# Kernel tuning notes

Measured on AMD Instinct MI355X. Metric: run time of the kernel, lower is better.

The kernel has to match this reference:

```python
import jax, jax.numpy as jnp
import numpy as np
from jax import lax

N = 63        # fixed by ConvTranspose chain: 3->5->9->17->33->63
ML = 3        # smoother mid channels
KS = 7        # smoother kernel size
MID = 32      # hypernet mid channels
K_ITERS = 5   # outer solver iterations
B = 256


def _conv2d(x, w, pad):
    return lax.conv_general_dilated(x, w, (1, 1), [(pad, pad), (pad, pad)],
                                    dimension_numbers=('NCHW', 'OIHW', 'NCHW'))


def _batch_conv2d(x, kernels):
    # per-sample 3x3 stencil conv via grouped conv: x [B,1,m,m], kernels [B,1,3,3]
    b, _, m1, m2 = x.shape
    out = lax.conv_general_dilated(x.reshape(1, b, m1, m2), kernels, (1, 1),
                                   [(0, 0), (0, 0)],
                                   dimension_numbers=('NCHW', 'OIHW', 'NCHW'),
                                   feature_group_count=b)
    return out.reshape(b, 1, m1 - 2, m2 - 2)


def _conv_transpose2d(x, w, b, stride, padding):
    # torch ConvTranspose2d: w layout [in, out, k, k]
    k = w.shape[-1]
    w2 = jnp.flip(w, (-2, -1)).transpose(1, 0, 2, 3)  # [out, in, k, k]
    p = k - 1 - padding
    y = lax.conv_general_dilated(x, w2, (1, 1), [(p, p), (p, p)],
                                 lhs_dilation=(stride, stride),
                                 dimension_numbers=('NCHW', 'OIHW', 'NCHW'))
    return y + b[None, :, None, None]


def _pad_bc(x):
    # F.pad (1,0,1,0) with 0 then (0,1,0,1) with 1
    x = jnp.pad(x, ((0, 0), (0, 0), (1, 0), (1, 0)))
    return jnp.pad(x, ((0, 0), (0, 0), (0, 1), (0, 1)), constant_values=1.0)


def _gelu(x):
    return jax.nn.gelu(x, approximate=False)  # torch nn.GELU default is exact


def setup_inputs() -> dict:
    key = jax.random.key(0)
    ks = jax.random.split(key, 24)
    s = 0.02
    d = {}
    d['x'] = jax.random.normal(ks[0], (B, 1, N, N), jnp.float32)
    d['f'] = jax.random.normal(ks[1], (B, 1, N, N), jnp.float32)
    d['kernelA'] = jax.random.normal(ks[2], (B, 1, 3, 3), jnp.float32)
    # smoother hypernetwork (two Linear(9->100->mL*ks*ks) stacks)
    d['fc1_w1'] = jax.random.normal(ks[3], (9, 100), jnp.float32) * s
    d['fc1_b1'] = jnp.zeros((100,), jnp.float32)
    d['fc1_w2'] = jax.random.normal(ks[4], (100, ML * KS * KS), jnp.float32) * s
    d['fc1_b2'] = jnp.zeros((ML * KS * KS,), jnp.float32)
    d['fc2_w1'] = jax.random.normal(ks[5], (9, 100), jnp.float32) * s
    d['fc2_b1'] = jnp.zeros((100,), jnp.float32)
    d['fc2_w2'] = jax.random.normal(ks[6], (100, ML * KS * KS), jnp.float32) * s
    d['fc2_b2'] = jnp.zeros((ML * KS * KS,), jnp.float32)
    # CNNFNS meta: 5 ConvTranspose2d layers (torch weight layout [in,out,k,k])
    d['ct1_w'] = jax.random.normal(ks[7], (1, MID, 3, 3), jnp.float32) * s
    d['ct1_b'] = jnp.zeros((MID,), jnp.float32)
    d['ct2_w'] = jax.random.normal(ks[8], (MID, MID, 3, 3), jnp.float32) * s
    d['ct2_b'] = jnp.zeros((MID,), jnp.float32)
    d['ct3_w'] = jax.random.normal(ks[9], (MID, MID, 3, 3), jnp.float32) * s
    d['ct3_b'] = jnp.zeros((MID,), jnp.float32)
    d['ct4_w'] = jax.random.normal(ks[10], (MID, MID, 3, 3), jnp.float32) * s
    d['ct4_b'] = jnp.zeros((MID,), jnp.float32)
    d['ct5_w'] = jax.random.normal(ks[11], (MID, 2, 3, 3), jnp.float32) * s
    d['ct5_b'] = jnp.zeros((2,), jnp.float32)
    return d


def reference(x, f, kernelA,
              fc1_w1, fc1_b1, fc1_w2, fc1_b2,
              fc2_w1, fc2_b1, fc2_w2, fc2_b2,
              ct1_w, ct1_b, ct2_w, ct2_b, ct3_w, ct3_b, ct4_w, ct4_b, ct5_w, ct5_b):
    bsz = x.shape[0]

    # --- hypernet weights depend only on kernelA: hoist out of the K loop ---
    flatA = kernelA.reshape(bsz, 9)
    w1 = (_gelu(flatA @ fc1_w1 + fc1_b1) @ fc1_w2 + fc1_b2).reshape(bsz, ML, 1, KS, KS)
    w2 = (_gelu(flatA @ fc2_w1 + fc2_b1) @ fc2_w2 + fc2_b2).reshape(bsz, 1, ML, KS, KS)

    h = _gelu(_conv_transpose2d(kernelA, ct1_w, ct1_b, 2, 1))
    h = _gelu(_conv_transpose2d(h, ct2_w, ct2_b, 2, 1))
    h = _gelu(_conv_transpose2d(h, ct3_w, ct3_b, 2, 1))
    h = _gelu(_conv_transpose2d(h, ct4_w, ct4_b, 2, 1))
    h = _conv_transpose2d(h, ct5_w, ct5_b, 2, 2)          # [B,2,N,N]
    hw = h.reshape(bsz, 1, N, N, 2)                        # memory-reinterp view as in torch
    wc = lax.complex(hw[..., 0], hw[..., 1])               # [B,1,N,N] complex

    def residual(xc):
        return f - _batch_conv2d(_pad_bc(xc), kernelA)

    def smoother(xc):
        r = residual(xc)
        def per(r_i, a_i, b_i):
            t = _conv2d(r_i[None], a_i, KS // 2)           # [1,ML,N,N]
            return _conv2d(t, b_i, KS // 2)[0]             # [1,N,N]
        g2 = jax.vmap(per)(r, w1, w2)
        return xc + g2

    def h_correct(r):
        r_hat = jnp.fft.fft2(r, norm='ortho')
        out_ft = r_hat * wc
        # torch irfft2(s=(N,N)) trims last dim to N//2+1
        return jnp.fft.irfft2(out_ft[..., : N // 2 + 1], s=(N, N), norm='ortho')

    for _ in range(K_ITERS):
        x = smoother(x)
        x = x + h_correct(residual(x))
    r = residual(x)
    return jnp.linalg.norm(r) / bsz
```

## Files before the change

### kernel.cpp

```cpp
#include <hip/hip_runtime.h>
#include <math.h>

#define NB   256
#define ND   63
#define NN   3969

__device__ __forceinline__ float gelu_f(float v){
    return 0.5f * v * (1.0f + erff(v * 0.70710678118654752440f));
}

#define FMA4(A, W, S) { (A).x=fmaf((W).x,(S),(A).x); (A).y=fmaf((W).y,(S),(A).y); \
                        (A).z=fmaf((W).z,(S),(A).z); (A).w=fmaf((W).w,(S),(A).w); }

union F4  { float4 v;    float a[4];  };
union W16 { float4 v[4]; float a[16]; };

__device__ __forceinline__ float4 gelu4(const F4& x){
    float4 r;
    r.x = gelu_f(x.a[0]); r.y = gelu_f(x.a[1]);
    r.z = gelu_f(x.a[2]); r.w = gelu_f(x.a[3]);
    return r;
}

__device__ __forceinline__ int dec_base(int uc, int H){
    int h2 = H >> 1;
    return (uc < h2) ? 4*uc : (uc < H) ? 4*(uc - h2) + 1 : 2*H;
}

template<int SIN, int SOUT, int OST>
__device__ __forceinline__ void ct_quad_stage(const float* __restrict__ cin,
                                              float* __restrict__ cout,
                                              const float* __restrict__ wb,
                                              const float* __restrict__ bsv,
                                              int tid){
    const int H  = (SOUT - 1) >> 1;
    const int UX = H + 1;
    const int NU = UX * UX * 8;
    for (int u = tid; u < NU; u += 512){
        const int cell = u >> 3, q = u & 7;
        const int ucy = cell / UX, ucx = cell - ucy*UX;
        const int oy = dec_base(ucy, H), ox = dec_base(ucx, H);
        const bool vx = (ox + 2 <= 2*H), vy = (oy + 2 <= 2*H);
        int nky, kyA[2], iyA[2];
        if (oy & 1){ nky=2; kyA[0]=0; iyA[0]=(oy+1)>>1; kyA[1]=2; iyA[1]=(oy-1)>>1; }
        else       { nky=1; kyA[0]=1; iyA[0]=oy>>1; kyA[1]=1; iyA[1]=0; }
        int nkx, kxA[2], ixA[2];
        if (ox & 1){ nkx=2; kxA[0]=0; ixA[0]=(ox+1)>>1; kxA[1]=2; ixA[1]=(ox-1)>>1; }
        else       { nkx=1; kxA[0]=1; ixA[0]=ox>>1; kxA[1]=1; ixA[1]=0; }
        F4 a00, a01, a10, a11;
        a00.v = ((const float4*)bsv)[q]; a01.v = a00.v; a10.v = a00.v; a11.v = a00.v;
        for (int yi = 0; yi < nky; yi++)
        for (int xi = 0; xi < nkx; xi++){
            const float* wp  = wb + (kyA[yi]*3 + kxA[xi])*1024 + 4*q;
            const float* p00 = cin + (iyA[yi]*SIN + ixA[xi])*36;
            const float* p01 = p00 + 36;
            const float* p10 = p00 + SIN*36;
            const float* p11 = p10 + 36;
            #pragma unroll
            for (int g = 0; g < 8; g++){
                F4 i00, i01, i10, i11;
                i00.v = *(const float4*)(p00 + 4*g);
                i01.v = *(const float4*)(p01 + 4*g);
                i10.v = *(const float4*)(p10 + 4*g);
                i11.v = *(const float4*)(p11 + 4*g);
                #pragma unroll
                for (int cc = 0; cc < 4; cc++){
                    float4 w = *(const float4*)(wp + (4*g + cc)*32);
                    FMA4(a00.v, w, i00.a[cc]);
                    FMA4(a01.v, w, i01.a[cc]);
                    FMA4(a10.v, w, i10.a[cc]);
                    FMA4(a11.v, w, i11.a[cc]);
                }
            }
        }
        float4 g00 = gelu4(a00), g01 = gelu4(a01), g10 = gelu4(a10), g11 = gelu4(a11);
        size_t base = (size_t)(oy*SOUT + ox)*OST + 4*q;
        *(float4*)(cout + base) = g00;
        if (vx)        *(float4*)(cout + base + 2*(size_t)OST) = g01;
        if (vy)        *(float4*)(cout + base + 2*(size_t)SOUT*OST) = g10;
        if (vx && vy)  *(float4*)(cout + base + 2*(size_t)(SOUT+1)*OST) = g11;
    }
}

__global__ __launch_bounds__(512) void k_ct1234(const float* __restrict__ kA,
                                                const float* __restrict__ cw1,
                                                const float* __restrict__ cw2,
                                                const float* __restrict__ cw3,
                                                const float* __restrict__ cw4,
                                                const float* __restrict__ b1,
                                                const float* __restrict__ b2,
                                                const float* __restrict__ b3,
                                                const float* __restrict__ b4,
                                                float* __restrict__ c4out,
                                                float* __restrict__ acc){
    __shared__ __align__(16) float wbuf[9216];
    __shared__ __align__(16) float w1s[288];
    __shared__ __align__(16) float c1s[31*36];
    __shared__ __align__(16) float c2s[91*36];
    __shared__ __align__(16) float c3s[307*36];
    __shared__ float b1s[32], b2s[32], b3s[32], b4s[32];
    const int b = blockIdx.x, tid = threadIdx.x;
    if (b == 0 && tid == 0) acc[0] = 0.f;
    for (int i = tid; i < 9216; i += 512){
        int ci = i / 288, co = (i / 9) & 31, tap = i % 9;
        wbuf[tap*1024 + ci*32 + co] = cw2[i];
    }
    if (tid < 288) w1s[(tid % 9)*32 + tid/9] = cw1[tid];
    if (tid < 32){ b1s[tid]=b1[tid]; b2s[tid]=b2[tid]; b3s[tid]=b3[tid]; b4s[tid]=b4[tid]; }
    __syncthreads();
    if (tid < 200){
        int px = tid >> 3, q = tid & 7;
        int oy = px / 5, ox = px % 5;
        F4 a4; a4.v = ((const float4*)b1s)[q];
        int nky, kyA[2], iyA[2];
        if (oy & 1){ nky=2; kyA[0]=0; iyA[0]=(oy+1)/2; kyA[1]=2; iyA[1]=(oy-1)/2; }
        else       { nky=1; kyA[0]=1; iyA[0]=oy/2; kyA[1]=1; iyA[1]=0; }
        int nkx, kxA[2], ixA[2];
        if (ox & 1){ nkx=2; kxA[0]=0; ixA[0]=(ox+1)/2; kxA[1]=2; ixA[1]=(ox-1)/2; }
        else       { nkx=1; kxA[0]=1; ixA[0]=ox/2; kxA[1]=1; ixA[1]=0; }
        const float* ab = kA + b*9;
        for (int yi = 0; yi < nky; yi++)
        for (int xi = 0; xi < nkx; xi++){
            float v = ab[iyA[yi]*3 + ixA[xi]];
            float4 w = *(const float4*)(w1s + (kyA[yi]*3 + kxA[xi])*32 + 4*q);
            FMA4(a4.v, w, v);
        }
        *(float4*)(c1s + px*36 + 4*q) = gelu4(a4);
    }
    __syncthreads();
    ct_quad_stage<5, 9, 36>(c1s, c2s, wbuf, b2s, tid);
    __syncthreads();
    for (int i = tid; i < 9216; i += 512){
        int ci = i / 288, co = (i / 9) & 31, tap = i % 9;
        wbuf[tap*1024 + ci*32 + co] = cw3[i];
    }
    __syncthreads();
    ct_quad_stage<9, 17, 36>(c2s, c3s, wbuf, b3s, tid);
    __syncthreads();
    for (int i = tid; i < 9216; i += 512){
        int ci = i / 288, co = (i / 9) & 31, tap = i % 9;
        wbuf[tap*1024 + ci*32 + co] = cw4[i];
    }
    __syncthreads();
    ct_quad_stage<17, 33, 32>(c3s, c4out + (size_t)b*(1089*32), wbuf, b4s, tid);
}

__global__ __launch_bounds__(512) void k_solve(const float* __restrict__ x0g,
                                               const float* __restrict__ f,
                                               const float* __restrict__ kAg,
                                               const float* __restrict__ w1a, const float* __restrict__ b1a,
                                               const float* __restrict__ w2a, const float* __restrict__ b2a,
                                               const float* __restrict__ w1b, const float* __restrict__ b1b,
                                               const float* __restrict__ w2b, const float* __restrict__ b2b,
                                               const float* __restrict__ cw5,
                                               const float* __restrict__ b5,
                                               const float* __restrict__ c4g,
                                               float* __restrict__ accg){
    __shared__ __align__(16) float xs[63*68 + 8];
    __shared__ __align__(16) float U[17152 + 8];
    __shared__ __align__(16) float Fs_r[4288];
    __shared__ __align__(16) float Fs_i[4288];
    __shared__ __align__(16) float vcs[4096];
    __shared__ float ws5b[576];
    __shared__ float w1s[148], w2s[148], dvs[64], ds_r[32], ds_i[32], red[8], hs[100];
    const int b = blockIdx.x, tid = threadIdx.x;
    float* rs  = U;
    float* tc0 = U + 4288;
    float* tc1 = U + 8576;
    float* tc2 = U + 12864;
    float*  rP  = U;
    const float4* rP4 = (const float4*)U;
    float2* TtC = (float2*)(U + 4096);
    float2* MC2 = (float2*)U;
    float4* CC4 = (float4*)(U + 4096);
    float* c5s = U;
    const float4* F4r = (const float4*)Fs_r;
    const float4* F4i = (const float4*)Fs_i;
    const float4* vc4s = (const float4*)vcs;
    const float* fg = f + (size_t)b*NN;
    float ka[9];
    #pragma unroll
    for (int i = 0; i < 9; i++) ka[i] = kAg[b*9 + i];

    for (int i = tid; i < 4288; i += 512){
        int r = i / 68, c = i % 68;
        float vr = 0.f, vi = 0.f;
        if (r < 63 && c < 63){
            int m = (r * c) % 63;
            float ang = 6.283185307179586f * (float)m / 63.0f;
            vr = cosf(ang); vi = -sinf(ang);
        }
        Fs_r[i] = vr; Fs_i[i] = vi;
    }
    for (int i = tid; i < 576; i += 512){
        int ci = i / 18, co = (i / 9) & 1, tap = i % 9;
        ws5b[tap*64 + ci*2 + co] = cw5[i];
    }
    for (int i = tid; i < NN; i += 512) xs[(i/ND)*68 + (i%ND)] = x0g[(size_t)b*NN + i];
    if (tid < 100){
        float s = b1a[tid];
        #pragma unroll
        for (int i = 0; i < 9; i++) s = fmaf(ka[i], w1a[i*100 + tid], s);
        hs[tid] = gelu_f(s);
    }
    __syncthreads();
    if (tid < 147){
        float s = b2a[tid];
        for (int k = 0; k < 100; k++) s = fmaf(hs[k], w2a[k*147 + tid], s);
        w1s[tid] = s;
    }
    __syncthreads();
    if (tid < 100){
        float s = b1b[tid];
        #pragma unroll
        for (int i = 0; i < 9; i++) s = fmaf(ka[i], w1b[i*100 + tid], s);
        hs[tid] = gelu_f(s);
    }
    __syncthreads();
    if (tid < 147){
        float s = b2b[tid];
        for (int k = 0; k < 100; k++) s = fmaf(hs[k], w2b[k*147 + tid], s);
        w2s[tid] = s;
    }
    {
        const float* ib = c4g + (size_t)b * (1089*32);
        float bb0 = b5[0], bb1 = b5[1];
        for (int p = tid; p < NN; p += 512){
            int oy = p / ND, ox = p % ND;
            float a0 = bb0, a1 = bb1;
            int nky, kyA[2], iyA[2];
            if ((oy & 1) == 0){ nky=2; kyA[0]=0; iyA[0]=oy/2+1; kyA[1]=2; iyA[1]=oy/2; }
            else              { nky=1; kyA[0]=1; iyA[0]=(oy+1)/2; kyA[1]=1; iyA[1]=0; }
            int nkx, kxA[2], ixA[2];
            if ((ox & 1) == 0){ nkx=2; kxA[0]=0; ixA[0]=ox/2+1; kxA[1]=2; ixA[1]=ox/2; }
            else              { nkx=1; kxA[0]=1; ixA[0]=(ox+1)/2; kxA[1]=1; ixA[1]=0; }
            for (int yi = 0; yi < nky; yi++)
            for (int xi = 0; xi < nkx; xi++){
                const float* ip = ib + ((size_t)iyA[yi]*33 + ixA[xi])*32;
                const float* wp = ws5b + (kyA[yi]*3 + kxA[xi])*64;
                #pragma unroll
                for (int g = 0; g < 8; g++){
                    F4 iv; iv.v = *(const float4*)(ip + 4*g);
                    #pragma unroll
                    for (int q = 0; q < 4; q++){
                        int ci = 4*g + q;
                        a0 = fmaf(iv.a[q], wp[ci*2],   a0);
                        a1 = fmaf(iv.a[q], wp[ci*2+1], a1);
                    }
                }
            }
            c5s[p]      = a0;
            c5s[NN + p] = a1;
        }
    }
    __syncthreads();
    {
        const float sc = 1.0f / 3969.0f;
        float4* vout = (float4*)vcs;
        for (int i = tid; i < 1024; i += 512){
            int ky = i >> 5, ct2 = i & 31;
            float4 o;
            #pragma unroll
            for (int j = 0; j < 2; j++){
                int kx = 2*ct2 + j;
                float re = 0.f, im = 0.f;
                if (kx <= 31){ int o2 = 2*(ky*ND + kx); re = c5s[o2]*sc; im = c5s[o2+1]*sc; }
                else if (kx <= 62){
                    int sy = (ND - ky) % ND, sx = ND - kx;
                    int o2 = 2*(sy*ND + sx); re = c5s[o2]*sc; im = -c5s[o2+1]*sc;
                }
                if (j == 0){ o.x = re; o.y = im; } else { o.z = re; o.w = im; }
            }
            vout[i] = o;
        }
        if (tid < 32){
            float2 d = {0.f, 0.f};
            if (tid >= 1){
                int iA = (ND - tid) * ND, iB = tid * ND;
                d.x = (c5s[2*iA]     - c5s[2*iB])     * sc;
                d.y = (c5s[2*iA + 1] + c5s[2*iB + 1]) * sc;
            }
            ((float2*)dvs)[tid] = d;
        }
    }
    __syncthreads();

    const int kt = tid >> 4, cg = tid & 15;

    for (int it = 0; it < 5; it++){
        for (int i = tid; i < NN; i += 512){
            int y = i / ND, xx = i % ND;
            float s = 0.f;
            #pragma unroll
            for (int dy = 0; dy < 3; dy++){
                int u = y + dy;
                #pragma unroll
                for (int dx = 0; dx < 3; dx++){
                    int v = xx + dx;
                    float p;
                    if (u == 64 || v == 64)    p = 1.0f;
                    else if (u == 0 || v == 0) p = 0.0f;
                    else                       p = xs[(u-1)*68 + (v-1)];
                    s = fmaf(p, ka[dy*3 + dx], s);
                }
            }
            rs[y*68 + 3 + xx] = fg[i] - s;
        }
        for (int i = tid; i < 1276; i += 512){
            int buf = i / 319, j = i - buf*319;
            float* base = U + buf*4288;
            int idx;
            if (j < 315){ int rr = j/5, cc = j - rr*5; idx = rr*68 + ((cc < 3) ? cc : 63 + cc); }
            else idx = 4284 + (j - 315);
            base[idx] = 0.f;
        }
        __syncthreads();
        const bool act = tid < 504;
        const int y0 = tid >> 3, x0c = 8*(tid & 7);
        if (act){
            float A0[8] = {}, A1[8] = {}, A2[8] = {};
            for (int dy = 0; dy < 7; dy++){
                int ry = y0 + dy - 3;
                if (ry < 0 || ry >= 63) continue;
                W16 w16;
                const float4* rp = (const float4*)(rs + ry*68 + x0c);
                w16.v[0]=rp[0]; w16.v[1]=rp[1]; w16.v[2]=rp[2]; w16.v[3]=rp[3];
                #pragma unroll
                for (int dx = 0; dx < 7; dx++){
                    float w0 = w1s[dy*7 + dx];
                    float w1 = w1s[49 + dy*7 + dx];
                    float w2 = w1s[98 + dy*7 + dx];
                    #pragma unroll
                    for (int t = 0; t < 8; t++){
                        float v = w16.a[t+dx];
                        A0[t] = fmaf(w0, v, A0[t]);
                        A1[t] = fmaf(w1, v, A1[t]);
                        A2[t] = fmaf(w2, v, A2[t]);
                    }
                }
            }
            int nw = 63 - x0c; if (nw > 8) nw = 8;
            for (int t = 0; t < nw; t++){
                int o = y0*68 + 3 + x0c + t;
                tc0[o] = A0[t]; tc1[o] = A1[t]; tc2[o] = A2[t];
            }
        }
        __syncthreads();
        if (act){
            float acc2[8] = {};
            #pragma unroll
            for (int c = 0; c < 3; c++){
                const float* tcc = (c == 0) ? tc0 : (c == 1) ? tc1 : tc2;
                for (int dy = 0; dy < 7; dy++){
                    int ry = y0 + dy - 3;
                    if (ry < 0 || ry >= 63) continue;
                    W16 w16;
                    const float4* tp = (const float4*)(tcc + ry*68 + x0c);
                    w16.v[0]=tp[0]; w16.v[1]=tp[1]; w16.v[2]=tp[2]; w16.v[3]=tp[3];
                    #pragma unroll
                    for (int dx = 0; dx < 7; dx++){
                        float wv = w2s[c*49 + dy*7 + dx];
                        #pragma unroll
                        for (int t = 0; t < 8; t++) acc2[t] = fmaf(wv, w16.a[t+dx], acc2[t]);
                    }
                }
            }
            int nw = 63 - x0c; if (nw > 8) nw = 8;
            for (int t = 0; t < nw; t++) xs[y0*68 + x0c + t] += acc2[t];
        }
        __syncthreads();
        for (int i = tid; i < 4096; i += 512){
            int y = i >> 6, xx = i & 63;
            float val = 0.f;
            if (y < 63 && xx < 63){
                float s = 0.f;
                #pragma unroll
                for (int dy = 0; dy < 3; dy++){
                    int u = y + dy;
                    #pragma unroll
                    for (int dx = 0; dx < 3; dx++){
                        int v = xx + dx;
                        float p;
                        if (u == 64 || v == 64)    p = 1.0f;
                        else if (u == 0 || v == 0) p = 0.0f;
                        else                       p = xs[(u-1)*68 + (v-1)];
                        s = fmaf(p, ka[dy*3 + dx], s);
                    }
                }
                val = fg[y*ND + xx] - s;
            }
            rP[i] = val;
        }
        __syncthreads();
        {
            float tr0=0.f,ti0=0.f,tr1=0.f,ti1=0.f,tr2=0.f,ti2=0.f,tr3=0.f,ti3=0.f;
            for (int mq = 0; mq < 16; mq++){
                F4 f4r, f4i;
                f4r.v = F4r[kt*17 + mq];
                f4i.v = F4i[kt*17 + mq];
                #pragma unroll
                for (int j = 0; j < 4; j++){
                    F4 rv; rv.v = rP4[(4*mq + j)*16 + cg];
                    float fr = f4r.a[j], fi = f4i.a[j];
                    tr0 = fmaf(fr, rv.a[0], tr0); ti0 = fmaf(fi, rv.a[0], ti0);
                    tr1 = fmaf(fr, rv.a[1], tr1); ti1 = fmaf(fi, rv.a[1], ti1);
                    tr2 = fmaf(fr, rv.a[2], tr2); ti2 = fmaf(fi, rv.a[2], ti2);
                    tr3 = fmaf(fr, rv.a[3], tr3); ti3 = fmaf(fi, rv.a[3], ti3);
                }
            }
            const int c0 = 4*cg;
            TtC[(c0+0)*32 + ((kt + c0 + 0) & 31)] = make_float2(tr0, ti0);
            TtC[(c0+1)*32 + ((kt + c0 + 1) & 31)] = make_float2(tr1, ti1);
            TtC[(c0+2)*32 + ((kt + c0 + 2) & 31)] = make_float2(tr2, ti2);
            TtC[(c0+3)*32 + ((kt + c0 + 3) & 31)] = make_float2(tr3, ti3);
        }
        __syncthreads();
        {
            float R0r,R0i,R1r,R1i,R2r,R2i,R3r,R3i;
            {
                float2 T0 = TtC[kt & 31];
                R0r = T0.x; R0i = T0.y;
                R1r = T0.x; R1i = T0.y;
                R2r = T0.x; R2i = T0.y;
                R3r = T0.x; R3i = T0.y;
            }
            for (int np = 1; np <= 31; np++){
                int n2 = 63 - np;
                float2 T1 = TtC[np*32 + ((kt + np) & 31)];
                float2 T2 = TtC[n2*32 + ((kt + n2) & 31)];
                F4 fr, fi;
                fr.v = F4r[np*17 + cg];
                fi.v = F4i[np*17 + cg];
                float Sx = T1.x + T2.x, Dx = T1.x - T2.x;
                float Sy = T1.y + T2.y, Dy = T2.y - T1.y;
                R0r = fmaf(fr.a[0], Sx, R0r); R0r = fmaf(fi.a[0], Dy, R0r);
                R0i = fmaf(fi.a[0], Dx, R0i); R0i = fmaf(fr.a[0], Sy, R0i);
                R1r = fmaf(fr.a[1], Sx, R1r); R1r = fmaf(fi.a[1], Dy, R1r);
                R1i = fmaf(fi.a[1], Dx, R1i); R1i = fmaf(fr.a[1], Sy, R1i);
                R2r = fmaf(fr.a[2], Sx, R2r); R2r = fmaf(fi.a[2], Dy, R2r);
                R2i = fmaf(fi.a[2], Dx, R2i); R2i = fmaf(fr.a[2], Sy, R2i);
                R3r = fmaf(fr.a[3], Sx, R3r); R3r = fmaf(fi.a[3], Dy, R3r);
                R3i = fmaf(fi.a[3], Dx, R3i); R3i = fmaf(fr.a[3], Sy, R3i);
            }
            if (cg == 0){
                float2 dv = ((const float2*)dvs)[kt];
                ds_r[kt] = R0r*dv.x + R0i*dv.y;
                ds_i[kt] = R0r*dv.y - R0i*dv.x;
            }
            float4 vA = vc4s[kt*32 + 2*cg];
            float4 vB = vc4s[kt*32 + 2*cg + 1];
            const int c0 = 4*cg, rot = kt;
            MC2[kt*64 + ((c0+0 + rot) & 63)] = make_float2(R0r*vA.x - R0i*vA.y, R0r*vA.y + R0i*vA.x);
            MC2[kt*64 + ((c0+1 + rot) & 63)] = make_float2(R1r*vA.z - R1i*vA.w, R1r*vA.w + R1i*vA.z);
            MC2[kt*64 + ((c0+2 + rot) & 63)] = make_float2(R2r*vB.x - R2i*vB.y, R2r*vB.y + R2i*vB.x);
            MC2[kt*64 + ((c0+3 + rot) & 63)] = make_float2(R3r*vB.z - R3i*vB.w, R3r*vB.w + R3i*vB.z);
        }
        __syncthreads();
        {
            const int rot = kt;
            float C0r,C0i,C1r,C1i,C2r,C2i,C3r,C3i;
            {
                float2 M0 = MC2[kt*64 + (rot & 63)];
                C0r = M0.x; C0i = M0.y;
                C1r = M0.x; C1i = M0.y;
                C2r = M0.x; C2i = M0.y;
                C3r = M0.x; C3i = M0.y;
            }
            for (int lp = 1; lp <= 31; lp++){
                int l2 = 63 - lp;
                float2 M1 = MC2[kt*64 + ((lp + rot) & 63)];
                float2 M2 = MC2[kt*64 + ((l2 + rot) & 63)];
                F4 fr, fi;
                fr.v = F4r[lp*17 + cg];
                fi.v = F4i[lp*17 + cg];
                float SMx = M1.x + M2.x, DMx = M2.x - M1.x;
                float SMy = M1.y + M2.y, DMy = M1.y - M2.y;
                C0r = fmaf(fr.a[0], SMx, C0r); C0r = fmaf(fi.a[0], DMy, C0r);
                C0i = fmaf(fr.a[0], SMy, C0i); C0i = fmaf(fi.a[0], DMx, C0i);
                C1r = fmaf(fr.a[1], SMx, C1r); C1r = fmaf(fi.a[1], DMy, C1r);
                C1i = fmaf(fr.a[1], SMy, C1i); C1i = fmaf(fi.a[1], DMx, C1i);
                C2r = fmaf(fr.a[2], SMx, C2r); C2r = fmaf(fi.a[2], DMy, C2r);
                C2i = fmaf(fr.a[2], SMy, C2i); C2i = fmaf(fi.a[2], DMx, C2i);
                C3r = fmaf(fr.a[3], SMx, C3r); C3r = fmaf(fi.a[3], DMy, C3r);
                C3i = fmaf(fr.a[3], SMy, C3i); C3i = fmaf(fi.a[3], DMx, C3i);
            }
            float sc2 = (kt == 0) ? 0.5f : 1.0f;
            CC4[kt*33 + 2*cg]     = make_float4(C0r*sc2, C0i*sc2, C1r*sc2, C1i*sc2);
            CC4[kt*33 + 2*cg + 1] = make_float4(C2r*sc2, C2i*sc2, C3r*sc2, C3i*sc2);
        }
        __syncthreads();
        if (tid < 256){
            const int pr = tid >> 3, qb = tid & 7;
            float sr[8] = {}, si[8] = {};
            float er = 0.f, ei = 0.f;
            for (int nq = 0; nq < 8; nq++){
                F4 f4r, f4i;
                f4r.v = F4r[pr*17 + nq];
                f4i.v = F4i[pr*17 + nq];
                #pragma unroll
                for (int j = 0; j < 4; j++){
                    int n = 4*nq + j;
                    float fr = f4r.a[j], fi = f4i.a[j];
                    float4 cA = CC4[n*33 + qb];
                    float4 cB = CC4[n*33 + qb + 8];
                    float4 cC = CC4[n*33 + qb + 16];
                    float4 cD = CC4[n*33 + qb + 24];
                    sr[0]=fmaf(fr,cA.x,sr[0]); si[0]=fmaf(fi,cA.y,si[0]);
                    sr[1]=fmaf(fr,cA.z,sr[1]); si[1]=fmaf(fi,cA.w,si[1]);
                    sr[2]=fmaf(fr,cB.x,sr[2]); si[2]=fmaf(fi,cB.y,si[2]);
                    sr[3]=fmaf(fr,cB.z,sr[3]); si[3]=fmaf(fi,cB.w,si[3]);
                    sr[4]=fmaf(fr,cC.x,sr[4]); si[4]=fmaf(fi,cC.y,si[4]);
                    sr[5]=fmaf(fr,cC.z,sr[5]); si[5]=fmaf(fi,cC.w,si[5]);
                    sr[6]=fmaf(fr,cD.x,sr[6]); si[6]=fmaf(fi,cD.y,si[6]);
                    sr[7]=fmaf(fr,cD.z,sr[7]); si[7]=fmaf(fi,cD.w,si[7]);
                    er = fmaf(fr, ds_r[n], er); ei = fmaf(fi, ds_i[n], ei);
                }
            }
            {
                float e0 = er - ei;
                float* xrow = xs + pr*68;
                float2* xp0 = (float2*)(xrow + 2*qb);
                float2* xp1 = (float2*)(xrow + 2*qb + 16);
                float2* xp2 = (float2*)(xrow + 2*qb + 32);
                float2* xp3 = (float2*)(xrow + 2*qb + 48);
                float2 v0=*xp0, v1=*xp1, v2=*xp2, v3=*xp3;
                v0.x += 2.f*(sr[0]+si[0]) + e0; v0.y += 2.f*(sr[1]+si[1]) + e0;
                v1.x += 2.f*(sr[2]+si[2]) + e0; v1.y += 2.f*(sr[3]+si[3]) + e0;
                v2.x += 2.f*(sr[4]+si[4]) + e0; v2.y += 2.f*(sr[5]+si[5]) + e0;
                v3.x += 2.f*(sr[6]+si[6]) + e0; v3.y += 2.f*(sr[7]+si[7]) + e0;
                *xp0=v0; *xp1=v1; *xp2=v2; *xp3=v3;
            }
            if (pr > 0){
                float e1 = er + ei;
                float* xrow = xs + (63-pr)*68;
                float2* xp0 = (float2*)(xrow + 2*qb);
                float2* xp1 = (float2*)(xrow + 2*qb + 16);
                float2* xp2 = (float2*)(xrow + 2*qb + 32);
                float2* xp3 = (float2*)(xrow + 2*qb + 48);
                float2 v0=*xp0, v1=*xp1, v2=*xp2, v3=*xp3;
                v0.x += 2.f*(sr[0]-si[0]) + e1; v0.y += 2.f*(sr[1]-si[1]) + e1;
                v1.x += 2.f*(sr[2]-si[2]) + e1; v1.y += 2.f*(sr[3]-si[3]) + e1;
                v2.x += 2.f*(sr[4]-si[4]) + e1; v2.y += 2.f*(sr[5]-si[5]) + e1;
                v3.x += 2.f*(sr[6]-si[6]) + e1; v3.y += 2.f*(sr[7]-si[7]) + e1;
                *xp0=v0; *xp1=v1; *xp2=v2; *xp3=v3;
            }
        }
        __syncthreads();
    }
    float s = 0.f;
    for (int i = tid; i < NN; i += 512){
        int y = i / ND, xx = i % ND;
        float cv = 0.f;
        #pragma unroll
        for (int dy = 0; dy < 3; dy++){
            int u = y + dy;
            #pragma unroll
            for (int dx = 0; dx < 3; dx++){
                int v = xx + dx;
                float p;
                if (u == 64 || v == 64)    p = 1.0f;
                else if (u == 0 || v == 0) p = 0.0f;
                else                       p = xs[(u-1)*68 + (v-1)];
                cv = fmaf(p, ka[dy*3 + dx], cv);
            }
        }
        float r = fg[i] - cv;
        s = fmaf(r, r, s);
    }
    #pragma unroll
    for (int off = 32; off > 0; off >>= 1) s += __shfl_down(s, off, 64);
    int lane = tid & 63, w = tid >> 6;
    if (lane == 0) red[w] = s;
    __syncthreads();
    if (tid == 0){
        float t = 0.f;
        #pragma unroll
        for (int i = 0; i < 8; i++) t += red[i];
        atomicAdd(accg, t);
    }
}

__global__ void k_final(const float* __restrict__ acc, float* __restrict__ out){
    if (threadIdx.x == 0 && blockIdx.x == 0) out[0] = sqrtf(acc[0]) * (1.0f/256.0f);
}

extern "C" void kernel_launch(void* const* d_in, const int* in_sizes, int n_in,
                              void* d_out, int out_size, void* d_ws, size_t ws_size,
                              hipStream_t stream){
    const float* x0     = (const float*)d_in[0];
    const float* f      = (const float*)d_in[1];
    const float* kA     = (const float*)d_in[2];
    const float* fc1_w1 = (const float*)d_in[3];
    const float* fc1_b1 = (const float*)d_in[4];
    const float* fc1_w2 = (const float*)d_in[5];
    const float* fc1_b2 = (const float*)d_in[6];
    const float* fc2_w1 = (const float*)d_in[7];
    const float* fc2_b1 = (const float*)d_in[8];
    const float* fc2_w2 = (const float*)d_in[9];
    const float* fc2_b2 = (const float*)d_in[10];
    const float* ct1_w  = (const float*)d_in[11];
    const float* ct1_b  = (const float*)d_in[12];
    const float* ct2_w  = (const float*)d_in[13];
    const float* ct2_b  = (const float*)d_in[14];
    const float* ct3_w  = (const float*)d_in[15];
    const float* ct3_b  = (const float*)d_in[16];
    const float* ct4_w  = (const float*)d_in[17];
    const float* ct4_b  = (const float*)d_in[18];
    const float* ct5_w  = (const float*)d_in[19];
    const float* ct5_b  = (const float*)d_in[20];
    float* out = (float*)d_out;

    float* ws = (float*)d_ws;
    size_t off = 0;
    auto take = [&](size_t n){ float* p = ws + off; off += (n + 63) & ~(size_t)63; return p; };
    float* acc = take(64);
    float* c4  = take((size_t)NB*32*1089);
    (void)ws_size; (void)in_sizes; (void)n_in; (void)out_size;

    k_ct1234<<<NB, 512, 0, stream>>>(kA, ct1_w, ct2_w, ct3_w, ct4_w,
                                     ct1_b, ct2_b, ct3_b, ct4_b, c4, acc);
    k_solve<<<NB, 512, 0, stream>>>(x0, f, kA,
                                    fc1_w1, fc1_b1, fc1_w2, fc1_b2,
                                    fc2_w1, fc2_b1, fc2_w2, fc2_b2,
                                    ct5_w, ct5_b, c4, acc);
    k_final<<<1, 64, 0, stream>>>(acc, out);
}
```

Baseline: 353.3 us.

## Pad solution tile with boundary halo and exploit row symmetry in DFT stage

Stores the solution in a shared buffer with a baked-in halo (zeros on top/left, ones on bottom/right), so the 3x3 residual stencils become branch-free, vectorized 8-wide register sweeps reusing float4 row loads. All residual computations, including the final norm, switch to this tiled form. The first DFT stage also pairs rows m and 63-m, using cos/sin symmetry to roughly halve its multiply-adds. The cost is a larger shared array and remapped indexing that must stay consistent with the halo layout.

```diff
diff --git a/kernel.cpp b/kernel.cpp
--- a/kernel.cpp
+++ b/kernel.cpp
@@ -156,7 +156,7 @@
                                                const float* __restrict__ b5,
                                                const float* __restrict__ c4g,
                                                float* __restrict__ accg){
-    __shared__ __align__(16) float xs[63*68 + 8];
+    __shared__ __align__(16) float xs[65*68 + 8];
     __shared__ __align__(16) float U[17152 + 8];
     __shared__ __align__(16) float Fs_r[4288];
     __shared__ __align__(16) float Fs_i[4288];
@@ -192,11 +192,16 @@
         }
         Fs_r[i] = vr; Fs_i[i] = vi;
     }
+    for (int i = tid; i < 4428; i += 512){
+        int r = i / 68, c = i - r*68;
+        bool interior = (r >= 1 && r <= 63 && c >= 4 && c <= 66);
+        if (!interior) xs[i] = (r == 64 || c == 67) ? 1.f : 0.f;
+    }
     for (int i = tid; i < 576; i += 512){
         int ci = i / 18, co = (i / 9) & 1, tap = i % 9;
         ws5b[tap*64 + ci*2 + co] = cw5[i];
     }
-    for (int i = tid; i < NN; i += 512) xs[(i/ND)*68 + (i%ND)] = x0g[(size_t)b*NN + i];
+    for (int i = tid; i < NN; i += 512) xs[(i/ND + 1)*68 + (i%ND) + 4] = x0g[(size_t)b*NN + i];
     if (tid < 100){
         float s = b1a[tid];
         #pragma unroll
@@ -286,25 +291,27 @@
     __syncthreads();
 
     const int kt = tid >> 4, cg = tid & 15;
+    const bool act = tid < 504;
+    const int y0 = tid >> 3, xc = 8*(tid & 7);
 
     for (int it = 0; it < 5; it++){
-        for (int i = tid; i < NN; i += 512){
-            int y = i / ND, xx = i % ND;
-            float s = 0.f;
+        if (act){
+            float racc[8] = {};
             #pragma unroll
             for (int dy = 0; dy < 3; dy++){
-                int u = y + dy;
+                W16 w;
+                const float4* rp = (const float4*)(xs + (y0 + dy)*68 + xc);
+                w.v[0]=rp[0]; w.v[1]=rp[1]; w.v[2]=rp[2]; w.v[3]=rp[3];
                 #pragma unroll
                 for (int dx = 0; dx < 3; dx++){
-                    int v = xx + dx;
-                    float p;
-                    if (u == 64 || v == 64)    p = 1.0f;
-                    else if (u == 0 || v == 0) p = 0.0f;
-                    else                       p = xs[(u-1)*68 + (v-1)];
-                    s = fmaf(p, ka[dy*3 + dx], s);
-                }
-            }
-            rs[y*68 + 3 + xx] = fg[i] - s;
+                    float kv = ka[dy*3 + dx];
+                    #pragma unroll
+                    for (int t = 0; t < 8; t++) racc[t] = fmaf(kv, w.a[3 + t + dx], racc[t]);
+                }
+            }
+            int nw = 63 - xc; if (nw > 8) nw = 8;
+            const float* fr_ = fg + y0*ND + xc;
+            for (int t = 0; t < nw; t++) rs[y0*68 + 3 + xc + t] = fr_[t] - racc[t];
         }
         for (int i = tid; i < 1276; i += 512){
             int buf = i / 319, j = i - buf*319;
@@ -315,15 +322,13 @@
             base[idx] = 0.f;
         }
         __syncthreads();
-        const bool act = tid < 504;
-        const int y0 = tid >> 3, x0c = 8*(tid & 7);
         if (act){
             float A0[8] = {}, A1[8] = {}, A2[8] = {};
             for (int dy = 0; dy < 7; dy++){
                 int ry = y0 + dy - 3;
                 if (ry < 0 || ry >= 63) continue;
                 W16 w16;
-                const float4* rp = (const float4*)(rs + ry*68 + x0c);
+                const float4* rp = (const float4*)(rs + ry*68 + xc);
                 w16.v[0]=rp[0]; w16.v[1]=rp[1]; w16.v[2]=rp[2]; w16.v[3]=rp[3];
                 #pragma unroll
                 for (int dx = 0; dx < 7; dx++){
@@ -339,9 +344,9 @@
                     }
                 }
             }
-            int nw = 63 - x0c; if (nw > 8) nw = 8;
+            int nw = 63 - xc; if (nw > 8) nw = 8;
             for (int t = 0; t < nw; t++){
-                int o = y0*68 + 3 + x0c + t;
+                int o = y0*68 + 3 + xc + t;
                 tc0[o] = A0[t]; tc1[o] = A1[t]; tc2[o] = A2[t];
             }
         }
@@ -355,7 +360,7 @@
                     int ry = y0 + dy - 3;
                     if (ry < 0 || ry >= 63) continue;
                     W16 w16;
-                    const float4* tp = (const float4*)(tcc + ry*68 + x0c);
+                    const float4* tp = (const float4*)(tcc + ry*68 + xc);
                     w16.v[0]=tp[0]; w16.v[1]=tp[1]; w16.v[2]=tp[2]; w16.v[3]=tp[3];
                     #pragma unroll
                     for (int dx = 0; dx < 7; dx++){
@@ -365,49 +370,63 @@
                     }
                 }
             }
-            int nw = 63 - x0c; if (nw > 8) nw = 8;
-            for (int t = 0; t < nw; t++) xs[y0*68 + x0c + t] += acc2[t];
-        }
-        __syncthreads();
-        for (int i = tid; i < 4096; i += 512){
-            int y = i >> 6, xx = i & 63;
-            float val = 0.f;
-            if (y < 63 && xx < 63){
-                float s = 0.f;
+            int nw = 63 - xc; if (nw > 8) nw = 8;
+            for (int t = 0; t < nw; t++) xs[(y0+1)*68 + 4 + xc + t] += acc2[t];
+        }
+        __syncthreads();
+        if (act){
+            float racc[8] = {};
+            #pragma unroll
+            for (int dy = 0; dy < 3; dy++){
+                W16 w;
+                const float4* rp = (const float4*)(xs + (y0 + dy)*68 + xc);
+                w.v[0]=rp[0]; w.v[1]=rp[1]; w.v[2]=rp[2]; w.v[3]=rp[3];
                 #pragma unroll
-                for (int dy = 0; dy < 3; dy++){
-                    int u = y + dy;
+                for (int dx = 0; dx < 3; dx++){
+                    float kv = ka[dy*3 + dx];
                     #pragma unroll
-                    for (int dx = 0; dx < 3; dx++){
-                        int v = xx + dx;
-                        float p;
-                        if (u == 64 || v == 64)    p = 1.0f;
-                        else if (u == 0 || v == 0) p = 0.0f;
-                        else                       p = xs[(u-1)*68 + (v-1)];
-                        s = fmaf(p, ka[dy*3 + dx], s);
-                    }
-                }
-                val = fg[y*ND + xx] - s;
-            }
-            rP[i] = val;
+                    for (int t = 0; t < 8; t++) racc[t] = fmaf(kv, w.a[3 + t + dx], racc[t]);
+                }
+            }
+            float out[8];
+            #pragma unroll
+            for (int t = 0; t < 8; t++){
+                int ci = xc + t; if (ci > 62) ci = 62;
+                float fv = fg[y0*ND + ci];
+                out[t] = (xc + t < 63) ? (fv - racc[t]) : 0.f;
+            }
+            *(float4*)(rP + y0*64 + xc)     = make_float4(out[0],out[1],out[2],out[3]);
+            *(float4*)(rP + y0*64 + xc + 4) = make_float4(out[4],out[5],out[6],out[7]);
         }
         __syncthreads();
         {
-            float tr0=0.f,ti0=0.f,tr1=0.f,ti1=0.f,tr2=0.f,ti2=0.f,tr3=0.f,ti3=0.f;
-            for (int mq = 0; mq < 16; mq++){
+            float tr0,ti0=0.f,tr1,ti1=0.f,tr2,ti2=0.f,tr3,ti3=0.f;
+            { F4 rv; rv.v = rP4[cg]; tr0=rv.a[0]; tr1=rv.a[1]; tr2=rv.a[2]; tr3=rv.a[3]; }
+            #define A_PAIR(MM, JJ) { \
+                F4 r1, r2; \
+                r1.v = rP4[(MM)*16 + cg]; \
+                r2.v = rP4[(63-(MM))*16 + cg]; \
+                float fr = f4r.a[JJ], fi = f4i.a[JJ]; \
+                float S0=r1.a[0]+r2.a[0], D0=r1.a[0]-r2.a[0]; \
+                float S1=r1.a[1]+r2.a[1], D1=r1.a[1]-r2.a[1]; \
+                float S2=r1.a[2]+r2.a[2], D2=r1.a[2]-r2.a[2]; \
+                float S3=r1.a[3]+r2.a[3], D3=r1.a[3]-r2.a[3]; \
+                tr0 = fmaf(fr, S0, tr0); ti0 = fmaf(fi, D0, ti0); \
+                tr1 = fmaf(fr, S1, tr1); ti1 = fmaf(fi, D1, ti1); \
+                tr2 = fmaf(fr, S2, tr2); ti2 = fmaf(fi, D2, ti2); \
+                tr3 = fmaf(fr, S3, tr3); ti3 = fmaf(fi, D3, ti3); }
+            {
+                F4 f4r, f4i; f4r.v = F4r[kt*17]; f4i.v = F4i[kt*17];
+                A_PAIR(1, 1) A_PAIR(2, 2) A_PAIR(3, 3)
+            }
+            for (int mq = 1; mq < 8; mq++){
                 F4 f4r, f4i;
                 f4r.v = F4r[kt*17 + mq];
                 f4i.v = F4i[kt*17 + mq];
-                #pragma unroll
-                for (int j = 0; j < 4; j++){
-                    F4 rv; rv.v = rP4[(4*mq + j)*16 + cg];
-                    float fr = f4r.a[j], fi = f4i.a[j];
-                    tr0 = fmaf(fr, rv.a[0], tr0); ti0 = fmaf(fi, rv.a[0], ti0);
-                    tr1 = fmaf(fr, rv.a[1], tr1); ti1 = fmaf(fi, rv.a[1], ti1);
-                    tr2 = fmaf(fr, rv.a[2], tr2); ti2 = fmaf(fi, rv.a[2], ti2);
-                    tr3 = fmaf(fr, rv.a[3], tr3); ti3 = fmaf(fi, rv.a[3], ti3);
-                }
-            }
+                A_PAIR(4*mq + 0, 0) A_PAIR(4*mq + 1, 1)
+                A_PAIR(4*mq + 2, 2) A_PAIR(4*mq + 3, 3)
+            }
+            #undef A_PAIR
             const int c0 = 4*cg;
             TtC[(c0+0)*32 + ((kt + c0 + 0) & 31)] = make_float2(tr0, ti0);
             TtC[(c0+1)*32 + ((kt + c0 + 1) & 31)] = make_float2(tr1, ti1);
@@ -518,7 +537,7 @@
             }
             {
                 float e0 = er - ei;
-                float* xrow = xs + pr*68;
+                float* xrow = xs + (pr+1)*68 + 4;
                 float2* xp0 = (float2*)(xrow + 2*qb);
                 float2* xp1 = (float2*)(xrow + 2*qb + 16);
                 float2* xp2 = (float2*)(xrow + 2*qb + 32);
@@ -532,7 +551,7 @@
             }
             if (pr > 0){
                 float e1 = er + ei;
-                float* xrow = xs + (63-pr)*68;
+                float* xrow = xs + (63-pr+1)*68 + 4;
                 float2* xp0 = (float2*)(xrow + 2*qb);
                 float2* xp1 = (float2*)(xrow + 2*qb + 16);
                 float2* xp2 = (float2*)(xrow + 2*qb + 32);
@@ -548,24 +567,27 @@
         __syncthreads();
     }
     float s = 0.f;
-    for (int i = tid; i < NN; i += 512){
-        int y = i / ND, xx = i % ND;
-        float cv = 0.f;
+    if (act){
+        float racc[8] = {};
         #pragma unroll
         for (int dy = 0; dy < 3; dy++){
-            int u = y + dy;
+            W16 w;
+            const float4* rp = (const float4*)(xs + (y0 + dy)*68 + xc);
+            w.v[0]=rp[0]; w.v[1]=rp[1]; w.v[2]=rp[2]; w.v[3]=rp[3];
             #pragma unroll
             for (int dx = 0; dx < 3; dx++){
-                int v = xx + dx;
-                float p;
-                if (u == 64 || v == 64)    p = 1.0f;
-                else if (u == 0 || v == 0) p = 0.0f;
-                else                       p = xs[(u-1)*68 + (v-1)];
-                cv = fmaf(p, ka[dy*3 + dx], cv);
-            }
-        }
-        float r = fg[i] - cv;
-        s = fmaf(r, r, s);
+                float kv = ka[dy*3 + dx];
+                #pragma unroll
+                for (int t = 0; t < 8; t++) racc[t] = fmaf(kv, w.a[3 + t + dx], racc[t]);
+            }
+        }
+        #pragma unroll
+        for (int t = 0; t < 8; t++){
+            if (xc + t < 63){
+                float r = fg[y0*ND + xc + t] - racc[t];
+                s = fmaf(r, r, s);
+            }
+        }
     }
     #pragma unroll
     for (int off = 32; off > 0; off >>= 1) s += __shfl_down(s, off, 64);
```

Measured after the change: 353.2 us. No clear change (-0.0%).
